# Optimization experiments

Hardware: AMD Instinct MI355X
Metric: run time of the kernel (lower is better)

The kernel has to match this reference:

```python
import jax, jax.numpy as jnp
import numpy as np

C = 8.0


def _linear_scan(alpha, xbeta):
    # h_t = alpha_t * h_{t-1} + xbeta_t, scan over time axis=1
    def combine(e1, e2):
        a1, b1 = e1
        a2, b2 = e2
        return a2 * a1, a2 * b1 + b2
    _, h = jax.lax.associative_scan(combine, (alpha, xbeta), axis=1)
    return h


def setup_inputs() -> dict:
    dim = 2048
    B, T = 4, 4096
    key = jax.random.key(0)
    k_x, k_wi, k_wg = jax.random.split(key, 3)
    std = dim ** -0.5
    x = jax.random.normal(k_x, (B, T, dim), dtype=jnp.float32)
    W_in = jax.random.normal(k_wi, (dim, dim), dtype=jnp.float32) * std
    b_in = jnp.zeros((dim,), dtype=jnp.float32)
    W_gate = jax.random.normal(k_wg, (dim, dim), dtype=jnp.float32) * std
    b_gate = jnp.zeros((dim,), dtype=jnp.float32)
    forget_lambda = jnp.linspace(-4.323, -9.0, dim, dtype=jnp.float32)
    return {"x": x, "W_in": W_in, "b_in": b_in, "W_gate": W_gate,
            "b_gate": b_gate, "forget_lambda": forget_lambda}


def reference(x, W_in, b_in, W_gate, b_gate, forget_lambda):
    # x: [B, T, D]
    input_gate = jnp.einsum('btd,ed->bte', x, W_in) + b_in
    recurrence_gate = jnp.einsum('btd,ed->bte', x, W_gate) + b_gate
    # alpha_t = exp(-C * softplus(lambda) * sigmoid(r_t))  per channel
    alpha = jnp.exp(-C * jax.nn.softplus(forget_lambda) * jax.nn.sigmoid(recurrence_gate))
    beta = jnp.sqrt(1.0 - alpha ** 2 + 1e-6)
    xbeta = beta * jax.nn.sigmoid(input_gate) * x
    return _linear_scan(alpha, xbeta)
```

## Files before the change

kernel.cpp:

```cpp
#include <hip/hip_runtime.h>

typedef unsigned short u16;
typedef unsigned int u32;

using bf16x8 = __attribute__((ext_vector_type(8))) __bf16;
using f32x4  = __attribute__((ext_vector_type(4))) float;
using u16x8  = __attribute__((ext_vector_type(8))) u16;

#define BB 4
#define TT 4096
#define DD 2048
#define MM 16384
#define KK 2048
#define NCHUNK 16
#define CLEN 256

__device__ __forceinline__ u16 f2bf(float f) {
    u32 u = __float_as_uint(f);
    u32 r = (u + 0x7FFFu + ((u >> 16) & 1u)) >> 16;
    return (u16)r;
}

__device__ __forceinline__ void gload_lds16(const void* g, void* l) {
    __builtin_amdgcn_global_load_lds(
        (const __attribute__((address_space(1))) void*)g,
        (__attribute__((address_space(3))) void*)l, 16, 0, 0);
}

__global__ __launch_bounds__(256) void cvt_kernel(const float* __restrict__ in,
                                                  u16* __restrict__ out, int n8) {
    int i = blockIdx.x * 256 + threadIdx.x;
    if (i >= n8) return;
    const f32x4* p = (const f32x4*)in + (size_t)i * 2;
    f32x4 a = p[0], b = p[1];
    u16x8 o;
    o[0] = f2bf(a[0]); o[1] = f2bf(a[1]); o[2] = f2bf(a[2]); o[3] = f2bf(a[3]);
    o[4] = f2bf(b[0]); o[5] = f2bf(b[1]); o[6] = f2bf(b[2]); o[7] = f2bf(b[3]);
    *((u16x8*)out + i) = o;
}

#define BMg 256
#define BNg 128
#define BKg 32
#define NT (KK / BKg)

__global__ __launch_bounds__(512, 2) void gemm_dual8(
    const u16* __restrict__ xb, const u16* __restrict__ wib, const u16* __restrict__ wgb,
    const float* __restrict__ b_in, const float* __restrict__ b_gate,
    const float* __restrict__ lam, u32* __restrict__ pair)
{
    __shared__ u16 As[4][BMg * BKg];
    __shared__ u16 Bs[4][2][BNg * BKg];

    const int tid = threadIdx.x;
    const int bid = blockIdx.x;
    const int cpx = gridDim.x >> 3;
    const int swz = (bid & 7) * cpx + (bid >> 3);
    const int et = swz & 15;
    const int mt = swz >> 4;
    const size_t m0 = (size_t)mt * BMg;
    const size_t e0 = (size_t)et * BNg;

    const int lane = tid & 63;
    const int wid = tid >> 6;
    const int wr = wid >> 2;
    const int wc = wid & 3;
    const int r15 = lane & 15;
    const int s4 = lane >> 4;

    const int srow = tid >> 2;
    const int sseg = (tid & 3) ^ ((tid >> 3) & 3);
    const int skp  = sseg << 3;

    const int koff = ((s4 ^ ((r15 >> 1) & 3)) << 3);

    const u16* gA0 = xb  + (m0 + srow) * KK + skp;
    const u16* gA1 = gA0 + (size_t)128 * KK;
    const u16* gI  = wib + (e0 + srow) * KK + skp;
    const u16* gG  = wgb + (e0 + srow) * KK + skp;

    int aoff[8], boff[2];
#pragma unroll
    for (int q = 0; q < 8; q++) aoff[q] = (wr * 128 + q * 16 + r15) * BKg + koff;
#pragma unroll
    for (int ni = 0; ni < 2; ni++) boff[ni] = (wc * 32 + ni * 16 + r15) * BKg + koff;

#define STAGE_A(t) do { int _b = (t) & 3; size_t _k = (size_t)(t) * BKg; \
        gload_lds16(gA0 + _k, &As[_b][tid * 8]); \
        gload_lds16(gA1 + _k, &As[_b][4096 + tid * 8]); } while (0)
#define STAGE_B(t) do { int _b = (t) & 3; size_t _k = (size_t)(t) * BKg; \
        gload_lds16(gI + _k, &Bs[_b][0][tid * 8]); \
        gload_lds16(gG + _k, &Bs[_b][1][tid * 8]); } while (0)

    f32x4 accI[8][2], accG[8][2];
#pragma unroll
    for (int i = 0; i < 8; i++)
#pragma unroll
        for (int j = 0; j < 2; j++) {
            accI[i][j] = (f32x4){0.f, 0.f, 0.f, 0.f};
            accG[i][j] = (f32x4){0.f, 0.f, 0.f, 0.f};
        }

    STAGE_A(0); STAGE_B(0);
    STAGE_A(1); STAGE_B(1);
    STAGE_A(2); STAGE_B(2);
    asm volatile("s_waitcnt vmcnt(8)" ::: "memory");
    __builtin_amdgcn_s_barrier();

#define PHASE0(t) do { \
        const u16* Ab = &As[(t) & 3][0]; \
        const u16* BiB = &Bs[(t) & 3][0][0]; \
        const u16* BgB = &Bs[(t) & 3][1][0]; \
        _Pragma("unroll") for (int q = 0; q < 4; q++) aF[q] = *(const bf16x8*)&Ab[aoff[q]]; \
        _Pragma("unroll") for (int ni = 0; ni < 2; ni++) { \
            bI[ni] = *(const bf16x8*)&BiB[boff[ni]]; \
            bG[ni] = *(const bf16x8*)&BgB[boff[ni]]; } \
    } while (0)
#define PHASE1(t) do { \
        const u16* Ab = &As[(t) & 3][0]; \
        _Pragma("unroll") for (int q = 0; q < 4; q++) aF[q] = *(const bf16x8*)&Ab[aoff[q + 4]]; \
    } while (0)
#define MFMA_BURST(base) do { \
        asm volatile("s_waitcnt lgkmcnt(0)" ::: "memory"); \
        __builtin_amdgcn_sched_barrier(0); \
        __builtin_amdgcn_s_setprio(1); \
        _Pragma("unroll") for (int q = 0; q < 4; q++) \
        _Pragma("unroll") for (int ni = 0; ni < 2; ni++) { \
            accI[q + (base)][ni] = __builtin_amdgcn_mfma_f32_16x16x32_bf16(aF[q], bI[ni], accI[q + (base)][ni], 0, 0, 0); \
            accG[q + (base)][ni] = __builtin_amdgcn_mfma_f32_16x16x32_bf16(aF[q], bG[ni], accG[q + (base)][ni], 0, 0, 0); } \
        __builtin_amdgcn_s_setprio(0); \
    } while (0)

    bf16x8 bI[2], bG[2], aF[4];

#pragma unroll 4
    for (int t = 0; t < NT - 3; ++t) {
        PHASE0(t);
        STAGE_A(t + 3);
        __builtin_amdgcn_s_barrier();
        MFMA_BURST(0);
        __builtin_amdgcn_s_barrier();
        PHASE1(t);
        STAGE_B(t + 3);
        __builtin_amdgcn_s_barrier();
        MFMA_BURST(4);
        asm volatile("s_waitcnt vmcnt(8)" ::: "memory");
        __builtin_amdgcn_s_barrier();
    }
#pragma unroll 1
    for (int t = NT - 3; t < NT; ++t) {
        PHASE0(t);
        __builtin_amdgcn_s_barrier();
        MFMA_BURST(0);
        __builtin_amdgcn_s_barrier();
        PHASE1(t);
        __builtin_amdgcn_s_barrier();
        MFMA_BURST(4);
        if (t == NT - 3) asm volatile("s_waitcnt vmcnt(4)" ::: "memory");
        else             asm volatile("s_waitcnt vmcnt(0)" ::: "memory");
        __builtin_amdgcn_s_barrier();
    }

    float spl[2], biv[2], bgv[2];
    size_t ecol[2];
#pragma unroll
    for (int ni = 0; ni < 2; ni++) {
        size_t e = e0 + wc * 32 + ni * 16 + r15;
        ecol[ni] = e;
        spl[ni] = 8.0f * log1pf(__expf(lam[e]));
        biv[ni] = b_in[e];
        bgv[ni] = b_gate[e];
    }
    const int rbase = s4 * 4;
#pragma unroll
    for (int mi = 0; mi < 8; mi++) {
#pragma unroll
        for (int r = 0; r < 4; r++) {
            size_t m = m0 + wr * 128 + mi * 16 + rbase + r;
#pragma unroll
            for (int ni = 0; ni < 2; ni++) {
                size_t e = ecol[ni];
                float ig = accI[mi][ni][r] + biv[ni];
                float rg = accG[mi][ni][r] + bgv[ni];
                float sigr = 1.f / (1.f + __expf(-rg));
                float g = spl[ni] * sigr;
                float beta = sqrtf(1.f - __expf(-2.f * g) + 1e-6f);
                float xv = __uint_as_float((u32)xb[m * KK + e] << 16);
                float xbeta = beta * (1.f / (1.f + __expf(-ig))) * xv;
                u32 pk = (u32)f2bf(g) | (((u32)f2bf(xbeta)) << 16);
                pair[m * DD + e] = pk;
            }
        }
    }
#undef STAGE_A
#undef STAGE_B
#undef PHASE0
#undef PHASE1
#undef MFMA_BURST
}

__global__ __launch_bounds__(256) void scanA(const u32* __restrict__ pair,
                                             float* __restrict__ aggG,
                                             float* __restrict__ aggB) {
    int gid = blockIdx.x * 256 + threadIdx.x;
    int e = gid & (DD - 1);
    int rest = gid >> 11;
    int b = rest & 3;
    int c = rest >> 2;
    const u32* p = pair + ((size_t)(b * TT + c * CLEN)) * DD + e;
    float gsum = 0.f, h = 0.f;
#pragma unroll 4
    for (int t = 0; t < CLEN; ++t) {
        u32 v = *p; p += DD;
        float gf = __uint_as_float(v << 16);
        float xbv = __uint_as_float(v & 0xFFFF0000u);
        gsum += gf;
        h = fmaf(__expf(-gf), h, xbv);
    }
    int idx = ((b * NCHUNK + c) << 11) | e;
    aggG[idx] = gsum;
    aggB[idx] = h;
}

__global__ __launch_bounds__(256) void scanB(const float* __restrict__ aggG,
                                             const float* __restrict__ aggB,
                                             float* __restrict__ carry) {
    int gid = blockIdx.x * 256 + threadIdx.x;
    int e = gid & (DD - 1);
    int b = gid >> 11;
    float h = 0.f;
#pragma unroll
    for (int c = 0; c < NCHUNK; ++c) {
        int idx = ((b * NCHUNK + c) << 11) | e;
        carry[idx] = h;
        h = fmaf(__expf(-aggG[idx]), h, aggB[idx]);
    }
}

__global__ __launch_bounds__(256) void scanC(const u32* __restrict__ pair,
                                             const float* __restrict__ carry,
                                             float* __restrict__ out) {
    int gid = blockIdx.x * 256 + threadIdx.x;
    int e = gid & (DD - 1);
    int rest = gid >> 11;
    int b = rest & 3;
    int c = rest >> 2;
    const u32* p = pair + ((size_t)(b * TT + c * CLEN)) * DD + e;
    float* o = out + ((size_t)(b * TT + c * CLEN)) * DD + e;
    float h = carry[((b * NCHUNK + c) << 11) | e];
#pragma unroll 4
    for (int t = 0; t < CLEN; ++t) {
        u32 v = *p; p += DD;
        float gf = __uint_as_float(v << 16);
        float xbv = __uint_as_float(v & 0xFFFF0000u);
        h = fmaf(__expf(-gf), h, xbv);
        *o = h; o += DD;
    }
}

extern "C" void kernel_launch(void* const* d_in, const int* in_sizes, int n_in,
                              void* d_out, int out_size, void* d_ws, size_t ws_size,
                              hipStream_t stream) {
    const float* x      = (const float*)d_in[0];
    const float* W_in   = (const float*)d_in[1];
    const float* b_in   = (const float*)d_in[2];
    const float* W_gate = (const float*)d_in[3];
    const float* b_gate = (const float*)d_in[4];
    const float* lam    = (const float*)d_in[5];
    float* out = (float*)d_out;

    char* ws = (char*)d_ws;
    u16* xb   = (u16*)(ws);
    u16* wib  = (u16*)(ws + 67108864);
    u16* wgb  = (u16*)(ws + 75497472);
    u32* pair = (u32*)(ws + 83886080);
    float* aggG  = (float*)(ws + 218103808);
    float* aggB  = (float*)(ws + 218628096);
    float* carry = (float*)(ws + 219152384);

    cvt_kernel<<<16384, 256, 0, stream>>>(x, xb, MM * KK / 8);
    cvt_kernel<<<2048, 256, 0, stream>>>(W_in, wib, DD * KK / 8);
    cvt_kernel<<<2048, 256, 0, stream>>>(W_gate, wgb, DD * KK / 8);
    gemm_dual8<<<(MM / BMg) * (DD / BNg), 512, 0, stream>>>(xb, wib, wgb, b_in, b_gate, lam, pair);
    scanA<<<BB * DD * NCHUNK / 256, 256, 0, stream>>>(pair, aggG, aggB);
    scanB<<<BB * DD / 256, 256, 0, stream>>>(aggG, aggB, carry);
    scanC<<<BB * DD * NCHUNK / 256, 256, 0, stream>>>(pair, carry, out);
}
```

Measured before the change: 436.3 us.

## Collapse GEMM main loop to one barrier per k-step with early LDS reads

Restructures the pipelined GEMM main loop so each k-step uses a single vmcnt wait and barrier instead of four barriers. All A and B fragment LDS reads for the step are issued up front into an enlarged register set, followed by the next global-to-LDS stages. Partial lgkmcnt waits then let the first MFMA burst start while the second half of the A reads is still in flight. This aims to cut barrier stalls and overlap LDS reads with MFMA, at the cost of more fragment registers and reliance on the 4-buffer ring for write-after-read safety.

```diff
diff --git a/kernel.cpp b/kernel.cpp
--- a/kernel.cpp
+++ b/kernel.cpp
@@ -104,10 +104,10 @@
     STAGE_A(0); STAGE_B(0);
     STAGE_A(1); STAGE_B(1);
     STAGE_A(2); STAGE_B(2);
-    asm volatile("s_waitcnt vmcnt(8)" ::: "memory");
-    __builtin_amdgcn_s_barrier();
-
-#define PHASE0(t) do { \
+
+    bf16x8 aF[8], bI[2], bG[2];
+
+#define READS8(t) do { \
         const u16* Ab = &As[(t) & 3][0]; \
         const u16* BiB = &Bs[(t) & 3][0][0]; \
         const u16* BgB = &Bs[(t) & 3][1][0]; \
@@ -116,49 +116,50 @@
             bI[ni] = *(const bf16x8*)&BiB[boff[ni]]; \
             bG[ni] = *(const bf16x8*)&BgB[boff[ni]]; } \
     } while (0)
-#define PHASE1(t) do { \
+#define READS4(t) do { \
         const u16* Ab = &As[(t) & 3][0]; \
-        _Pragma("unroll") for (int q = 0; q < 4; q++) aF[q] = *(const bf16x8*)&Ab[aoff[q + 4]]; \
+        _Pragma("unroll") for (int q = 4; q < 8; q++) aF[q] = *(const bf16x8*)&Ab[aoff[q]]; \
     } while (0)
-#define MFMA_BURST(base) do { \
-        asm volatile("s_waitcnt lgkmcnt(0)" ::: "memory"); \
-        __builtin_amdgcn_sched_barrier(0); \
+#define BURST(base) do { \
         __builtin_amdgcn_s_setprio(1); \
         _Pragma("unroll") for (int q = 0; q < 4; q++) \
         _Pragma("unroll") for (int ni = 0; ni < 2; ni++) { \
-            accI[q + (base)][ni] = __builtin_amdgcn_mfma_f32_16x16x32_bf16(aF[q], bI[ni], accI[q + (base)][ni], 0, 0, 0); \
-            accG[q + (base)][ni] = __builtin_amdgcn_mfma_f32_16x16x32_bf16(aF[q], bG[ni], accG[q + (base)][ni], 0, 0, 0); } \
+            accI[q + (base)][ni] = __builtin_amdgcn_mfma_f32_16x16x32_bf16(aF[q + (base)], bI[ni], accI[q + (base)][ni], 0, 0, 0); \
+            accG[q + (base)][ni] = __builtin_amdgcn_mfma_f32_16x16x32_bf16(aF[q + (base)], bG[ni], accG[q + (base)][ni], 0, 0, 0); } \
         __builtin_amdgcn_s_setprio(0); \
     } while (0)
 
-    bf16x8 bI[2], bG[2], aF[4];
-
 #pragma unroll 4
     for (int t = 0; t < NT - 3; ++t) {
-        PHASE0(t);
-        STAGE_A(t + 3);
-        __builtin_amdgcn_s_barrier();
-        MFMA_BURST(0);
-        __builtin_amdgcn_s_barrier();
-        PHASE1(t);
-        STAGE_B(t + 3);
-        __builtin_amdgcn_s_barrier();
-        MFMA_BURST(4);
         asm volatile("s_waitcnt vmcnt(8)" ::: "memory");
         __builtin_amdgcn_s_barrier();
+        READS8(t);
+        asm volatile("" ::: "memory");
+        READS4(t);
+        STAGE_A(t + 3);
+        STAGE_B(t + 3);
+        asm volatile("s_waitcnt lgkmcnt(4)" ::: "memory");
+        __builtin_amdgcn_sched_barrier(0);
+        BURST(0);
+        asm volatile("s_waitcnt lgkmcnt(0)" ::: "memory");
+        __builtin_amdgcn_sched_barrier(0);
+        BURST(4);
     }
 #pragma unroll 1
     for (int t = NT - 3; t < NT; ++t) {
-        PHASE0(t);
+        if (t == NT - 3)      asm volatile("s_waitcnt vmcnt(8)" ::: "memory");
+        else if (t == NT - 2) asm volatile("s_waitcnt vmcnt(4)" ::: "memory");
+        else                  asm volatile("s_waitcnt vmcnt(0)" ::: "memory");
         __builtin_amdgcn_s_barrier();
-        MFMA_BURST(0);
-        __builtin_amdgcn_s_barrier();
-        PHASE1(t);
-        __builtin_amdgcn_s_barrier();
-        MFMA_BURST(4);
-        if (t == NT - 3) asm volatile("s_waitcnt vmcnt(4)" ::: "memory");
-        else             asm volatile("s_waitcnt vmcnt(0)" ::: "memory");
-        __builtin_amdgcn_s_barrier();
+        READS8(t);
+        asm volatile("" ::: "memory");
+        READS4(t);
+        asm volatile("s_waitcnt lgkmcnt(4)" ::: "memory");
+        __builtin_amdgcn_sched_barrier(0);
+        BURST(0);
+        asm volatile("s_waitcnt lgkmcnt(0)" ::: "memory");
+        __builtin_amdgcn_sched_barrier(0);
+        BURST(4);
     }
 
     float spl[2], biv[2], bgv[2];
@@ -194,9 +195,9 @@
     }
 #undef STAGE_A
 #undef STAGE_B
-#undef PHASE0
-#undef PHASE1
-#undef MFMA_BURST
+#undef READS8
+#undef READS4
+#undef BURST
 }
 
 __global__ __launch_bounds__(256) void scanA(const u32* __restrict__ pair,
```

New measurement: 462.9 us. 1.06x slower.

## Double-buffer GEMM fragments in registers and cut barriers to one per k-step

Applied to the files above, without the earlier changes.

The GEMM main loop becomes a two-step unrolled STEP macro that ping-pongs B fragments between two register sets. It also prefetches the next k-tile's A and B LDS fragments while the current MFMA burst runs, using partial lgkmcnt waits instead of full drains. Four s_barriers per k-step drop to one, and the separate tail loop is folded in by guarding the global stages. This is meant to hide LDS read latency behind MFMA work and cut synchronisation stalls, at the cost of more registers and tighter wait-count correctness (the last step reads an unused buffer).

```diff
diff --git a/kernel.cpp b/kernel.cpp
--- a/kernel.cpp
+++ b/kernel.cpp
@@ -104,61 +104,65 @@
     STAGE_A(0); STAGE_B(0);
     STAGE_A(1); STAGE_B(1);
     STAGE_A(2); STAGE_B(2);
-    asm volatile("s_waitcnt vmcnt(8)" ::: "memory");
+    asm volatile("s_waitcnt vmcnt(4)" ::: "memory");
     __builtin_amdgcn_s_barrier();
 
-#define PHASE0(t) do { \
-        const u16* Ab = &As[(t) & 3][0]; \
-        const u16* BiB = &Bs[(t) & 3][0][0]; \
-        const u16* BgB = &Bs[(t) & 3][1][0]; \
-        _Pragma("unroll") for (int q = 0; q < 4; q++) aF[q] = *(const bf16x8*)&Ab[aoff[q]]; \
-        _Pragma("unroll") for (int ni = 0; ni < 2; ni++) { \
-            bI[ni] = *(const bf16x8*)&BiB[boff[ni]]; \
-            bG[ni] = *(const bf16x8*)&BgB[boff[ni]]; } \
-    } while (0)
-#define PHASE1(t) do { \
-        const u16* Ab = &As[(t) & 3][0]; \
-        _Pragma("unroll") for (int q = 0; q < 4; q++) aF[q] = *(const bf16x8*)&Ab[aoff[q + 4]]; \
-    } while (0)
-#define MFMA_BURST(base) do { \
-        asm volatile("s_waitcnt lgkmcnt(0)" ::: "memory"); \
+    bf16x8 aq0[4], aq1[4], bIA[2], bGA[2], bIB[2], bGB[2];
+
+    {
+        const u16* Ab = &As[0][0];
+        const u16* Bi = &Bs[0][0][0];
+        const u16* Bg = &Bs[0][1][0];
+#pragma unroll
+        for (int q = 0; q < 4; q++) aq0[q] = *(const bf16x8*)&Ab[aoff[q]];
+#pragma unroll
+        for (int ni = 0; ni < 2; ni++) {
+            bIA[ni] = *(const bf16x8*)&Bi[boff[ni]];
+            bGA[ni] = *(const bf16x8*)&Bg[boff[ni]];
+        }
+    }
+
+#define STEP(t, bIc, bGc, bIn, bGn) do { \
+         \
+        { const u16* Ab = &As[(t) & 3][0]; \
+          _Pragma("unroll") for (int q = 0; q < 4; q++) \
+              aq1[q] = *(const bf16x8*)&Ab[aoff[q + 4]]; } \
+        if ((t) < NT - 3) STAGE_A((t) + 3); \
+        asm volatile("s_waitcnt lgkmcnt(4)" ::: "memory");  \
         __builtin_amdgcn_sched_barrier(0); \
         __builtin_amdgcn_s_setprio(1); \
         _Pragma("unroll") for (int q = 0; q < 4; q++) \
         _Pragma("unroll") for (int ni = 0; ni < 2; ni++) { \
-            accI[q + (base)][ni] = __builtin_amdgcn_mfma_f32_16x16x32_bf16(aF[q], bI[ni], accI[q + (base)][ni], 0, 0, 0); \
-            accG[q + (base)][ni] = __builtin_amdgcn_mfma_f32_16x16x32_bf16(aF[q], bG[ni], accG[q + (base)][ni], 0, 0, 0); } \
+            accI[q][ni] = __builtin_amdgcn_mfma_f32_16x16x32_bf16(aq0[q], bIc[ni], accI[q][ni], 0, 0, 0); \
+            accG[q][ni] = __builtin_amdgcn_mfma_f32_16x16x32_bf16(aq0[q], bGc[ni], accG[q][ni], 0, 0, 0); } \
         __builtin_amdgcn_s_setprio(0); \
+         \
+        { const u16* Ab2 = &As[((t) + 1) & 3][0]; \
+          const u16* Bi2 = &Bs[((t) + 1) & 3][0][0]; \
+          const u16* Bg2 = &Bs[((t) + 1) & 3][1][0]; \
+          _Pragma("unroll") for (int q = 0; q < 4; q++) \
+              aq0[q] = *(const bf16x8*)&Ab2[aoff[q]]; \
+          _Pragma("unroll") for (int ni = 0; ni < 2; ni++) { \
+              bIn[ni] = *(const bf16x8*)&Bi2[boff[ni]]; \
+              bGn[ni] = *(const bf16x8*)&Bg2[boff[ni]]; } } \
+        if ((t) < NT - 3) STAGE_B((t) + 3); \
+        asm volatile("s_waitcnt lgkmcnt(8)" ::: "memory");  \
+        __builtin_amdgcn_sched_barrier(0); \
+        __builtin_amdgcn_s_setprio(1); \
+        _Pragma("unroll") for (int q = 0; q < 4; q++) \
+        _Pragma("unroll") for (int ni = 0; ni < 2; ni++) { \
+            accI[q + 4][ni] = __builtin_amdgcn_mfma_f32_16x16x32_bf16(aq1[q], bIc[ni], accI[q + 4][ni], 0, 0, 0); \
+            accG[q + 4][ni] = __builtin_amdgcn_mfma_f32_16x16x32_bf16(aq1[q], bGc[ni], accG[q + 4][ni], 0, 0, 0); } \
+        __builtin_amdgcn_s_setprio(0); \
+        if ((t) < NT - 3) asm volatile("s_waitcnt vmcnt(4)" ::: "memory"); \
+        else              asm volatile("s_waitcnt vmcnt(0)" ::: "memory"); \
+        __builtin_amdgcn_s_barrier(); \
     } while (0)
 
-    bf16x8 bI[2], bG[2], aF[4];
-
-#pragma unroll 4
-    for (int t = 0; t < NT - 3; ++t) {
-        PHASE0(t);
-        STAGE_A(t + 3);
-        __builtin_amdgcn_s_barrier();
-        MFMA_BURST(0);
-        __builtin_amdgcn_s_barrier();
-        PHASE1(t);
-        STAGE_B(t + 3);
-        __builtin_amdgcn_s_barrier();
-        MFMA_BURST(4);
-        asm volatile("s_waitcnt vmcnt(8)" ::: "memory");
-        __builtin_amdgcn_s_barrier();
-    }
-#pragma unroll 1
-    for (int t = NT - 3; t < NT; ++t) {
-        PHASE0(t);
-        __builtin_amdgcn_s_barrier();
-        MFMA_BURST(0);
-        __builtin_amdgcn_s_barrier();
-        PHASE1(t);
-        __builtin_amdgcn_s_barrier();
-        MFMA_BURST(4);
-        if (t == NT - 3) asm volatile("s_waitcnt vmcnt(4)" ::: "memory");
-        else             asm volatile("s_waitcnt vmcnt(0)" ::: "memory");
-        __builtin_amdgcn_s_barrier();
+#pragma unroll 2
+    for (int t = 0; t < NT; t += 2) {
+        STEP(t,     bIA, bGA, bIB, bGB);
+        STEP(t + 1, bIB, bGB, bIA, bGA);
     }
 
     float spl[2], biv[2], bgv[2];
@@ -194,9 +198,7 @@
     }
 #undef STAGE_A
 #undef STAGE_B
-#undef PHASE0
-#undef PHASE1
-#undef MFMA_BURST
+#undef STEP
 }
 
 __global__ __launch_bounds__(256) void scanA(const u32* __restrict__ pair,
```

New measurement: 439.4 us. About the same (+0.7%).
